# Optimization experiments

Measured on AMD Instinct MI355X. Metric: run time of the kernel, lower is better.

Reference implementation:

```python
import jax, jax.numpy as jnp
import numpy as np

B, S, D, H = 4, 2048, 512, 8
DH = D // H  # head dim = 64
NEG = -1000000.0


def setup_inputs() -> dict:
    key = jax.random.key(0)
    ks = jax.random.split(key, 13)
    s = 1.0 / np.sqrt(D)
    return {
        "Q": jax.random.normal(ks[0], (B, S, D), jnp.float32),
        "K": jax.random.normal(ks[1], (B, S, D), jnp.float32),
        "V": jax.random.normal(ks[2], (B, S, D), jnp.float32),
        "Wq": jax.random.normal(ks[3], (D, D), jnp.float32) * s,
        "bq": jnp.zeros((D,), jnp.float32),
        "Wk": jax.random.normal(ks[4], (D, D), jnp.float32) * s,
        "bk": jnp.zeros((D,), jnp.float32),
        "Wv": jax.random.normal(ks[5], (D, D), jnp.float32) * s,
        "bv": jnp.zeros((D,), jnp.float32),
        "Wo": jax.random.normal(ks[6], (D, D), jnp.float32) * s,
        "bo": jnp.zeros((D,), jnp.float32),
        "masked": jax.random.randint(ks[7], (B,), 1, S + 1, jnp.int64),
    }


def _heads(x):
    # [B,S,D] -> [B,H,S,DH]
    return x.reshape(B, S, H, DH).transpose(0, 2, 1, 3)


def reference(Q, K, V, Wq, bq, Wk, bk, Wv, bv, Wo, bo, masked):
    q = _heads(Q @ Wq.T + bq)
    k = _heads(K @ Wk.T + bk)
    v = _heads(V @ Wv.T + bv)
    scores = jnp.einsum("bhqd,bhkd->bhqk", q, k) / jnp.sqrt(jnp.asarray(DH, q.dtype))
    # valid-length key mask, per batch (same for every head and query row)
    key_mask = jnp.arange(S)[None, None, None, :] < masked[:, None, None, None]
    scores = jnp.where(key_mask, scores, jnp.asarray(NEG, scores.dtype))
    weights = jax.nn.softmax(scores, axis=-1)
    out = jnp.einsum("bhqk,bhkd->bhqd", weights, v)  # [B,H,S,DH]
    out = out.transpose(0, 2, 1, 3).reshape(B, S, D)
    return out @ Wo.T + bo
```

## Files before the change

### kernel.cpp

```cpp
#include <hip/hip_runtime.h>
#include <stdint.h>


typedef __attribute__((ext_vector_type(8))) short short8;
typedef __attribute__((ext_vector_type(4))) short short4v;
typedef __attribute__((ext_vector_type(4))) float f32x4;
typedef __attribute__((ext_vector_type(4))) unsigned short u16x4;

#define MFMA16(a, b, c) __builtin_amdgcn_mfma_f32_16x16x32_bf16(a, b, c, 0, 0, 0)

#define SCALE_LOG2 0.18033688011112042f
#define FIXED_M    32.0f
#define MASKED_E2  -200.0f

__device__ __forceinline__ unsigned short f2bf(float f) {
    unsigned int x = __float_as_uint(f);
    unsigned int r = (x + 0x7fffu + ((x >> 16) & 1u)) >> 16;
    return (unsigned short)r;
}
__device__ __forceinline__ short8 load8(const unsigned short* p) {
    return *reinterpret_cast<const short8*>(p);
}
__device__ __forceinline__ void gload_lds16(const unsigned short* g, unsigned short* l) {
    __builtin_amdgcn_global_load_lds(
        (const __attribute__((address_space(1))) unsigned int*)g,
        (__attribute__((address_space(3))) unsigned int*)l, 16, 0, 0);
}

__global__ __launch_bounds__(256)
void convert_bf16(const float4* __restrict__ Q, const float4* __restrict__ K,
                  const float4* __restrict__ V, const float4* __restrict__ Wq,
                  const float4* __restrict__ Wk, const float4* __restrict__ Wv,
                  const float4* __restrict__ Wo, u16x4* __restrict__ dst)
{
    const int n = 3407872;
    for (int i = blockIdx.x * 256 + threadIdx.x; i < n; i += gridDim.x * 256) {
        const float4* src; int off;
        if      (i < 1048576) { src = Q;  off = i; }
        else if (i < 2097152) { src = K;  off = i - 1048576; }
        else if (i < 3145728) { src = V;  off = i - 2097152; }
        else if (i < 3211264) { src = Wq; off = i - 3145728; }
        else if (i < 3276800) { src = Wk; off = i - 3211264; }
        else if (i < 3342336) { src = Wv; off = i - 3276800; }
        else                  { src = Wo; off = i - 3342336; }
        const float4 v = src[off];
        u16x4 r;
        r[0] = f2bf(v.x); r[1] = f2bf(v.y); r[2] = f2bf(v.z); r[3] = f2bf(v.w);
        dst[i] = r;
    }
}

__global__ __launch_bounds__(256)
void gemm_bf(const unsigned short* __restrict__ Aall,
             const unsigned short* __restrict__ Wall,
             const float* __restrict__ b0, const float* __restrict__ b1,
             const float* __restrict__ b2,
             void* __restrict__ outall, int out_mode)
{
    __shared__ unsigned short As[128 * 64];
    __shared__ unsigned short Bs[128 * 64];

    const int z = blockIdx.y;
    const unsigned short* A = Aall + (long)z * 4194304;
    const unsigned short* W = Wall + z * 262144;
    const float* bias = (z == 0) ? b0 : (z == 1) ? b1 : b2;
    void* out = (out_mode == 0)
        ? (void*)((unsigned short*)outall + (long)z * 4194304) : outall;

    const int f    = blockIdx.x;
    const int xcd  = f & 7;
    const int slot = f >> 3;
    const int col0 = (slot & 3) * 128;
    const int row0 = ((slot >> 2) * 8 + xcd) * 128;

    const int tid  = threadIdx.x;
    const int lane = tid & 63;
    const int w    = tid >> 6;
    const int quad = lane >> 4;
    const int nlow = lane & 15;
    const int wm   = w >> 1, wn = w & 1;

    const unsigned short* ag[4];
    const unsigned short* wg[4];
    unsigned short *la[4], *lb[4];
#pragma unroll
    for (int i = 0; i < 4; i++) {
        const int s = i * 256 + tid;
        const int r = s >> 3, kcl = s & 7;
        const int kg = kcl ^ (r & 7);
        ag[i] = A + (long)(row0 + r) * 512 + kg * 8;
        wg[i] = W + (long)(col0 + r) * 512 + kg * 8;
        const int ldso = i * 2048 + ((tid >> 6) << 9);
        la[i] = As + ldso;
        lb[i] = Bs + ldso;
    }

    f32x4 acc[4][4];
#pragma unroll
    for (int t = 0; t < 4; t++)
#pragma unroll
        for (int g = 0; g < 4; g++) acc[t][g] = (f32x4){0.f, 0.f, 0.f, 0.f};

    for (int k0 = 0; k0 < 512; k0 += 64) {
#pragma unroll
        for (int i = 0; i < 4; i++) {
            gload_lds16(ag[i] + k0, la[i]);
            gload_lds16(wg[i] + k0, lb[i]);
        }
        __syncthreads();

        short8 af[4][2], bf[4][2];
#pragma unroll
        for (int t = 0; t < 4; t++) {
            const int rowa = wm * 64 + t * 16 + nlow;
            const int rowb = wn * 64 + t * 16 + nlow;
#pragma unroll
            for (int kc = 0; kc < 2; kc++) {
                const int c = (kc * 4 + quad) ^ (nlow & 7);
                af[t][kc] = load8(&As[(rowa * 8 + c) * 8]);
                bf[t][kc] = load8(&Bs[(rowb * 8 + c) * 8]);
            }
        }
#pragma unroll
        for (int kc = 0; kc < 2; kc++)
#pragma unroll
            for (int t = 0; t < 4; t++)
#pragma unroll
                for (int g = 0; g < 4; g++)
                    acc[t][g] = MFMA16(af[t][kc], bf[g][kc], acc[t][g]);
        __syncthreads();
    }

#pragma unroll
    for (int g = 0; g < 4; g++) {
        const int j = col0 + wn * 64 + g * 16 + nlow;
        const float bj = bias[j];
#pragma unroll
        for (int t = 0; t < 4; t++) {
#pragma unroll
            for (int r = 0; r < 4; r++) {
                const int i = row0 + wm * 64 + t * 16 + quad * 4 + r;
                const float v = acc[t][g][r] + bj;
                if (out_mode == 0) {
                    const int b = i >> 11, s = i & 2047;
                    const int h = j >> 6, dh = j & 63;
                    ((unsigned short*)out)[(((b * 8 + h) * 2048) + s) * 64 + dh] = f2bf(v);
                } else {
                    ((float*)out)[(long)i * 512 + j] = v;
                }
            }
        }
    }
}

__global__ __launch_bounds__(256)
void attn_kernel(const unsigned short* __restrict__ qp,
                 const unsigned short* __restrict__ kp,
                 const unsigned short* __restrict__ vp,
                 const void* __restrict__ masked,
                 unsigned short* __restrict__ out)
{
    __shared__ unsigned short Ks[32][72];
    __shared__ unsigned short Vt[64][40];
    __shared__ unsigned short Ps[4][16][44];

    const int tid  = threadIdx.x;
    const int lane = tid & 63;
    const int w    = tid >> 6;
    const int quad = lane >> 4;
    const int nlow = lane & 15;

    const int b  = blockIdx.z;
    const int h  = blockIdx.y;
    const int q0 = blockIdx.x * 64 + w * 16;
    const long base = ((long)(b * 8 + h)) * 2048 * 64;

    const long long first = *reinterpret_cast<const long long*>(masked);
    int kmax;
    if ((first >> 32) != 0) kmax = reinterpret_cast<const int*>(masked)[b];
    else                    kmax = (int)reinterpret_cast<const long long*>(masked)[b];
    kmax = min(max(kmax, 1), 2048);

    const unsigned short* qrow = qp + base + (long)(q0 + nlow) * 64;
    const short8 aq0 = load8(qrow + quad * 8);
    const short8 aq1 = load8(qrow + 32 + quad * 8);

    short8 ones;
#pragma unroll
    for (int j = 0; j < 8; j++) ones[j] = (short)0x3F80;

    f32x4 o_acc[4], lacc;
#pragma unroll
    for (int vb = 0; vb < 4; vb++) o_acc[vb] = (f32x4){0.f, 0.f, 0.f, 0.f};
    lacc = (f32x4){0.f, 0.f, 0.f, 0.f};

    const int srow = tid >> 3;
    const int skk  = (tid & 7) * 8;
    const int kg   = srow >> 3;
    const int ko   = srow & 7;
    const int nkt  = (kmax + 31) >> 5;

    for (int kt = 0; kt < nkt; kt++) {
        const int k0 = kt * 32;
        *reinterpret_cast<short8*>(&Ks[srow][skk]) =
            load8(&kp[base + (long)(k0 + srow) * 64 + skk]);
        short8 vv = load8(&vp[base + (long)(k0 + srow) * 64 + skk]);
#pragma unroll
        for (int j = 0; j < 8; j++) {
            const int dh = skk + j;
            Vt[dh][((kg ^ ((dh >> 3) & 3)) << 3) + ko] = (unsigned short)vv[j];
        }
        __syncthreads();

        f32x4 sacc[2];
        sacc[0] = (f32x4){0.f, 0.f, 0.f, 0.f};
        sacc[1] = (f32x4){0.f, 0.f, 0.f, 0.f};
#pragma unroll
        for (int kb = 0; kb < 2; kb++) {
            short8 bk0 = load8(&Ks[kb * 16 + nlow][quad * 8]);
            short8 bk1 = load8(&Ks[kb * 16 + nlow][32 + quad * 8]);
            sacc[kb] = MFMA16(aq0, bk0, sacc[kb]);
            sacc[kb] = MFMA16(aq1, bk1, sacc[kb]);
        }

#pragma unroll
        for (int kb = 0; kb < 2; kb++) {
            const bool valid = (k0 + kb * 16 + nlow) < kmax;
#pragma unroll
            for (int r = 0; r < 4; r++) {
                const float e = valid ? fmaf(sacc[kb][r], SCALE_LOG2, -FIXED_M)
                                      : MASKED_E2;
                Ps[w][quad * 4 + r][kb * 16 + nlow] = f2bf(exp2f(e));
            }
        }
        __threadfence_block();

        const short4v apl = *reinterpret_cast<const short4v*>(&Ps[w][nlow][quad * 8]);
        const short4v aph = *reinterpret_cast<const short4v*>(&Ps[w][nlow][quad * 8 + 4]);
        short8 ap;
        ap[0] = apl[0]; ap[1] = apl[1]; ap[2] = apl[2]; ap[3] = apl[3];
        ap[4] = aph[0]; ap[5] = aph[1]; ap[6] = aph[2]; ap[7] = aph[3];

        lacc = MFMA16(ap, ones, lacc);
#pragma unroll
        for (int vb = 0; vb < 4; vb++) {
            const int dhr = vb * 16 + nlow;
            short8 bv = load8(&Vt[dhr][(quad ^ ((dhr >> 3) & 3)) << 3]);
            o_acc[vb] = MFMA16(ap, bv, o_acc[vb]);
        }
        __syncthreads();
    }

    float inv_l[4];
#pragma unroll
    for (int r = 0; r < 4; r++) inv_l[r] = 1.0f / lacc[r];
#pragma unroll
    for (int vb = 0; vb < 4; vb++) {
#pragma unroll
        for (int r = 0; r < 4; r++) {
            const int s   = q0 + quad * 4 + r;
            const int col = h * 64 + vb * 16 + nlow;
            out[(long)(b * 2048 + s) * 512 + col] = f2bf(o_acc[vb][r] * inv_l[r]);
        }
    }
}

extern "C" void kernel_launch(void* const* d_in, const int* in_sizes, int n_in,
                              void* d_out, int out_size, void* d_ws, size_t ws_size,
                              hipStream_t stream)
{
    const float4* Q  = (const float4*)d_in[0];
    const float4* K  = (const float4*)d_in[1];
    const float4* V  = (const float4*)d_in[2];
    const float4* Wq = (const float4*)d_in[3];
    const float*  bq = (const float*)d_in[4];
    const float4* Wk = (const float4*)d_in[5];
    const float*  bk = (const float*)d_in[6];
    const float4* Wv = (const float4*)d_in[7];
    const float*  bv = (const float*)d_in[8];
    const float4* Wo = (const float4*)d_in[9];
    const float*  bo = (const float*)d_in[10];
    const void*   masked = d_in[11];

    unsigned short* ws16 = (unsigned short*)d_ws;
    unsigned short* QKVb = ws16;
    unsigned short* Wb   = ws16 + 12582912;
    unsigned short* qp   = ws16 + 13631488;
    unsigned short* kp   = qp + 4194304;
    unsigned short* vp   = kp + 4194304;
    unsigned short* ao   = ws16;

    convert_bf16<<<2048, 256, 0, stream>>>(Q, K, V, Wq, Wk, Wv, Wo, (u16x4*)ws16);
    gemm_bf<<<dim3(256, 3), 256, 0, stream>>>(QKVb, Wb, bq, bk, bv, qp, 0);
    attn_kernel<<<dim3(32, 8, 4), 256, 0, stream>>>(qp, kp, vp, masked, ao);
    gemm_bf<<<dim3(256, 1), 256, 0, stream>>>(ao, Wb + 3 * 262144, bo, bo, bo,
                                              d_out, 1);
}
```

Before: 186.4 us.

## Double-buffer K/V tiles with async LDS loads and 64-key steps in attention

The attention kernel now processes 64 keys per iteration instead of 32 and double-buffers the K and V tiles in shared memory. K goes to LDS through global_load_lds, and the next V tile is loaded into registers before the compute and transposed into LDS afterwards, so global loads overlap the MFMA work and there is one barrier per iteration. The LDS layouts switch to XOR swizzles to avoid bank conflicts, launch bounds now request 4 blocks per CU, and the grid is flattened with heads innermost. The costs are more LDS and registers per block, which could limit occupancy, and extra index arithmetic.

```diff
diff --git a/kernel.cpp b/kernel.cpp
--- a/kernel.cpp
+++ b/kernel.cpp
@@ -3,7 +3,6 @@
 
 
 typedef __attribute__((ext_vector_type(8))) short short8;
-typedef __attribute__((ext_vector_type(4))) short short4v;
 typedef __attribute__((ext_vector_type(4))) float f32x4;
 typedef __attribute__((ext_vector_type(4))) unsigned short u16x4;
 
@@ -153,16 +152,26 @@
     }
 }
 
-__global__ __launch_bounds__(256)
+__device__ __forceinline__ int ks_idx(int key, int dchunk) {
+    return key * 64 + ((dchunk ^ (key & 7)) << 3);
+}
+__device__ __forceinline__ int vt_idx(int key, int dh) {
+    return dh * 64 + ((((key >> 3) ^ (dh & 7) ^ ((dh >> 3) & 7)) << 3) + (key & 7));
+}
+__device__ __forceinline__ int ps_idx(int q, int key) {
+    return q * 64 + ((((key >> 3) ^ (q & 7)) << 3) + (key & 7));
+}
+
+__global__ __launch_bounds__(256, 4)
 void attn_kernel(const unsigned short* __restrict__ qp,
                  const unsigned short* __restrict__ kp,
                  const unsigned short* __restrict__ vp,
                  const void* __restrict__ masked,
                  unsigned short* __restrict__ out)
 {
-    __shared__ unsigned short Ks[32][72];
-    __shared__ unsigned short Vt[64][40];
-    __shared__ unsigned short Ps[4][16][44];
+    __shared__ unsigned short Ks[2][4096];
+    __shared__ unsigned short Vt[2][4096];
+    __shared__ unsigned short Ps[4][1024];
 
     const int tid  = threadIdx.x;
     const int lane = tid & 63;
@@ -170,9 +179,11 @@
     const int quad = lane >> 4;
     const int nlow = lane & 15;
 
-    const int b  = blockIdx.z;
-    const int h  = blockIdx.y;
-    const int q0 = blockIdx.x * 64 + w * 16;
+    const int f  = blockIdx.x;
+    const int h  = f & 7;
+    const int qb = (f >> 3) & 31;
+    const int b  = f >> 8;
+    const int q0 = qb * 64 + w * 16;
     const long base = ((long)(b * 8 + h)) * 2048 * 64;
 
     const long long first = *reinterpret_cast<const long long*>(masked);
@@ -180,6 +191,7 @@
     if ((first >> 32) != 0) kmax = reinterpret_cast<const int*>(masked)[b];
     else                    kmax = (int)reinterpret_cast<const long long*>(masked)[b];
     kmax = min(max(kmax, 1), 2048);
+    const int nkt = (kmax + 63) >> 6;
 
     const unsigned short* qrow = qp + base + (long)(q0 + nlow) * 64;
     const short8 aq0 = load8(qrow + quad * 8);
@@ -194,61 +206,95 @@
     for (int vb = 0; vb < 4; vb++) o_acc[vb] = (f32x4){0.f, 0.f, 0.f, 0.f};
     lacc = (f32x4){0.f, 0.f, 0.f, 0.f};
 
-    const int srow = tid >> 3;
-    const int skk  = (tid & 7) * 8;
-    const int kg   = srow >> 3;
-    const int ko   = srow & 7;
-    const int nkt  = (kmax + 31) >> 5;
+    const int kr0 = tid >> 3;
+    const int kr1 = 32 + kr0;
+    const unsigned short* kg0 = kp + base + (long)kr0 * 64 + (((tid & 7) ^ (kr0 & 7)) << 3);
+    const unsigned short* kg1 = kp + base + (long)kr1 * 64 + (((tid & 7) ^ (kr1 & 7)) << 3);
+    const int kd0 = (w << 9);
+    const int kd1 = 2048 + (w << 9);
+    const int vk0 = tid >> 3;
+    const int vk1 = 32 + vk0;
+    const int vd0 = (tid & 7) << 3;
+    const unsigned short* vg0 = vp + base + (long)vk0 * 64 + vd0;
+    const unsigned short* vg1 = vp + base + (long)vk1 * 64 + vd0;
+
+    gload_lds16(kg0, &Ks[0][kd0]);
+    gload_lds16(kg1, &Ks[0][kd1]);
+    {
+        short8 v0 = load8(vg0);
+        short8 v1 = load8(vg1);
+#pragma unroll
+        for (int j = 0; j < 8; j++) {
+            Vt[0][vt_idx(vk0, vd0 + j)] = (unsigned short)v0[j];
+            Vt[0][vt_idx(vk1, vd0 + j)] = (unsigned short)v1[j];
+        }
+    }
+    __syncthreads();
+
+    unsigned short* Psw = Ps[w];
+    int cur = 0;
+    short8 vv0, vv1;
 
     for (int kt = 0; kt < nkt; kt++) {
-        const int k0 = kt * 32;
-        *reinterpret_cast<short8*>(&Ks[srow][skk]) =
-            load8(&kp[base + (long)(k0 + srow) * 64 + skk]);
-        short8 vv = load8(&vp[base + (long)(k0 + srow) * 64 + skk]);
-#pragma unroll
-        for (int j = 0; j < 8; j++) {
-            const int dh = skk + j;
-            Vt[dh][((kg ^ ((dh >> 3) & 3)) << 3) + ko] = (unsigned short)vv[j];
-        }
-        __syncthreads();
-
-        f32x4 sacc[2];
-        sacc[0] = (f32x4){0.f, 0.f, 0.f, 0.f};
-        sacc[1] = (f32x4){0.f, 0.f, 0.f, 0.f};
-#pragma unroll
-        for (int kb = 0; kb < 2; kb++) {
-            short8 bk0 = load8(&Ks[kb * 16 + nlow][quad * 8]);
-            short8 bk1 = load8(&Ks[kb * 16 + nlow][32 + quad * 8]);
+        const int k0 = kt * 64;
+        const bool more = (kt + 1 < nkt);
+        if (more) {
+            const long off = (long)(k0 + 64) * 64;
+            gload_lds16(kg0 + off, &Ks[cur ^ 1][kd0]);
+            gload_lds16(kg1 + off, &Ks[cur ^ 1][kd1]);
+            vv0 = load8(vg0 + off);
+            vv1 = load8(vg1 + off);
+        }
+        const unsigned short* Ksc = Ks[cur];
+        const unsigned short* Vtc = Vt[cur];
+
+        f32x4 sacc[4];
+#pragma unroll
+        for (int kb = 0; kb < 4; kb++) sacc[kb] = (f32x4){0.f, 0.f, 0.f, 0.f};
+#pragma unroll
+        for (int kb = 0; kb < 4; kb++) {
+            const int key = kb * 16 + nlow;
+            short8 bk0 = load8(Ksc + ks_idx(key, quad));
+            short8 bk1 = load8(Ksc + ks_idx(key, 4 + quad));
             sacc[kb] = MFMA16(aq0, bk0, sacc[kb]);
             sacc[kb] = MFMA16(aq1, bk1, sacc[kb]);
         }
 
 #pragma unroll
-        for (int kb = 0; kb < 2; kb++) {
+        for (int kb = 0; kb < 4; kb++) {
             const bool valid = (k0 + kb * 16 + nlow) < kmax;
 #pragma unroll
             for (int r = 0; r < 4; r++) {
+                const int q = quad * 4 + r;
                 const float e = valid ? fmaf(sacc[kb][r], SCALE_LOG2, -FIXED_M)
                                       : MASKED_E2;
-                Ps[w][quad * 4 + r][kb * 16 + nlow] = f2bf(exp2f(e));
+                Psw[ps_idx(q, kb * 16 + nlow)] = f2bf(exp2f(e));
             }
         }
         __threadfence_block();
 
-        const short4v apl = *reinterpret_cast<const short4v*>(&Ps[w][nlow][quad * 8]);
-        const short4v aph = *reinterpret_cast<const short4v*>(&Ps[w][nlow][quad * 8 + 4]);
-        short8 ap;
-        ap[0] = apl[0]; ap[1] = apl[1]; ap[2] = apl[2]; ap[3] = apl[3];
-        ap[4] = aph[0]; ap[5] = aph[1]; ap[6] = aph[2]; ap[7] = aph[3];
-
-        lacc = MFMA16(ap, ones, lacc);
-#pragma unroll
-        for (int vb = 0; vb < 4; vb++) {
-            const int dhr = vb * 16 + nlow;
-            short8 bv = load8(&Vt[dhr][(quad ^ ((dhr >> 3) & 3)) << 3]);
-            o_acc[vb] = MFMA16(ap, bv, o_acc[vb]);
+#pragma unroll
+        for (int h2 = 0; h2 < 2; h2++) {
+            const int g = h2 * 4 + quad;
+            short8 ap = load8(Psw + ps_idx(nlow, g << 3));
+            lacc = MFMA16(ap, ones, lacc);
+#pragma unroll
+            for (int vb = 0; vb < 4; vb++) {
+                short8 bv = load8(Vtc + vt_idx(g << 3, vb * 16 + nlow));
+                o_acc[vb] = MFMA16(ap, bv, o_acc[vb]);
+            }
+        }
+
+        if (more) {
+            unsigned short* Vtn = Vt[cur ^ 1];
+#pragma unroll
+            for (int j = 0; j < 8; j++) {
+                Vtn[vt_idx(vk0, vd0 + j)] = (unsigned short)vv0[j];
+                Vtn[vt_idx(vk1, vd0 + j)] = (unsigned short)vv1[j];
+            }
         }
         __syncthreads();
+        cur ^= 1;
     }
 
     float inv_l[4];
@@ -292,7 +338,7 @@
 
     convert_bf16<<<2048, 256, 0, stream>>>(Q, K, V, Wq, Wk, Wv, Wo, (u16x4*)ws16);
     gemm_bf<<<dim3(256, 3), 256, 0, stream>>>(QKVb, Wb, bq, bk, bv, qp, 0);
-    attn_kernel<<<dim3(32, 8, 4), 256, 0, stream>>>(qp, kp, vp, masked, ao);
+    attn_kernel<<<dim3(1024), 256, 0, stream>>>(qp, kp, vp, masked, ao);
     gemm_bf<<<dim3(256, 1), 256, 0, stream>>>(ao, Wb + 3 * 262144, bo, bo, bo,
                                               d_out, 1);
 }
```

After: 176.2 us. 1.06x faster.
